# Kernel tuning notes

Measured on AMD Instinct MI355X. Metric: run time of the kernel, lower is better.

## Reference

```python
import jax, jax.numpy as jnp
import numpy as np

N_QUBITS = 8
INPUT_DIM = 256
SEQ_LEN = 256
BATCH = 512


def qgate(theta, x):
    # Closed-form expectation of the PennyLane circuit:
    #   RX(x_i) then RY(theta_i) on each wire (from |0>), then CNOT chain 0->1->...->n-1,
    #   measure <Z_k>.  Single-wire <Z_j> = cos(x_j) * cos(theta_j); CNOT chain maps
    #   Z_k -> Z_0 Z_1 ... Z_k in the Heisenberg picture, so on the product state
    #   <Z_k> = prod_{j<=k} cos(x_j) cos(theta_j).
    # x: (B, n_wires), theta: (n_wires,)
    return jnp.cumprod(jnp.cos(x) * jnp.cos(theta), axis=-1)


def setup_inputs() -> dict:
    key = jax.random.key(0)
    ks = jax.random.split(key, 14)
    d_in = INPUT_DIM + N_QUBITS  # concat([x, hx]) -> 264
    lin_scale = 1.0 / np.sqrt(d_in)
    inp = {
        "inputs": jax.random.normal(ks[0], (SEQ_LEN, BATCH, INPUT_DIM), dtype=jnp.float32),
        "Wf": jax.random.normal(ks[1], (N_QUBITS, d_in), dtype=jnp.float32) * lin_scale,
        "bf": jax.random.normal(ks[2], (N_QUBITS,), dtype=jnp.float32) * lin_scale,
        "Wi": jax.random.normal(ks[3], (N_QUBITS, d_in), dtype=jnp.float32) * lin_scale,
        "bi": jax.random.normal(ks[4], (N_QUBITS,), dtype=jnp.float32) * lin_scale,
        "Wu": jax.random.normal(ks[5], (N_QUBITS, d_in), dtype=jnp.float32) * lin_scale,
        "bu": jax.random.normal(ks[6], (N_QUBITS,), dtype=jnp.float32) * lin_scale,
        "Wo": jax.random.normal(ks[7], (N_QUBITS, d_in), dtype=jnp.float32) * lin_scale,
        "bo": jax.random.normal(ks[8], (N_QUBITS,), dtype=jnp.float32) * lin_scale,
        "pf": jax.random.normal(ks[9], (N_QUBITS,), dtype=jnp.float32),
        "pi_": jax.random.normal(ks[10], (N_QUBITS,), dtype=jnp.float32),
        "pu": jax.random.normal(ks[11], (N_QUBITS,), dtype=jnp.float32),
        "po": jax.random.normal(ks[12], (N_QUBITS,), dtype=jnp.float32),
    }
    return inp


def reference(inputs, Wf, bf, Wi, bi, Wu, bu, Wo, bo, pf, pi_, pu, po):
    B = inputs.shape[1]
    H = pf.shape[0]  # hidden_dim == n_qubits

    def step(carry, x):
        hx, cx = carry
        comb = jnp.concatenate([x, hx], axis=1)  # (B, input_dim + H)
        f = jax.nn.sigmoid(qgate(pf, comb @ Wf.T + bf))
        i = jax.nn.sigmoid(qgate(pi_, comb @ Wi.T + bi))
        g = jnp.tanh(qgate(pu, comb @ Wu.T + bu))
        o = jax.nn.sigmoid(qgate(po, comb @ Wo.T + bo))
        cx = f * cx + i * g
        hx = o * jnp.tanh(cx)
        return (hx, cx), hx

    init = (jnp.zeros((B, H), dtype=inputs.dtype), jnp.zeros((B, H), dtype=inputs.dtype))
    (hx, cx), stacked = jax.lax.scan(step, init, inputs)
    return stacked, hx, cx
```

## Files before the change

### kernel.cpp

```cpp
#include <hip/hip_runtime.h>
#include <hip/hip_bf16.h>


#define SEQ   256
#define BATCH 512
#define DIN   256
#define NROWS (SEQ * BATCH)
#define DCOMB 264
#define CHT   64
#define NCH   (SEQ / CHT)
#define ZBSTR 130
#define ZBUFSZ (32 * ZBSTR + 16)
#define HLSTR 260
#define INV2PI 0.15915494309189535f

typedef __attribute__((ext_vector_type(8))) short short8;
typedef __attribute__((ext_vector_type(4))) float f32x4;
typedef __attribute__((ext_vector_type(2))) float f32x2;

__device__ __forceinline__ short f2bf(float f) {
    union { __hip_bfloat16 h; short s; } u;
    u.h = __float2bfloat16(f);
    return u.s;
}
__device__ __forceinline__ float bf2f(short s) {
    union { short s; __hip_bfloat16 h; } u;
    u.s = s;
    return __bfloat162float(u.h);
}

__device__ __forceinline__ short8 pack8(float4 a, float4 b) {
    union { short8 s8; int i[4]; } u;
    union { __hip_bfloat162 h; int i; } v;
    v.h = __float22bfloat162_rn(make_float2(a.x, a.y)); u.i[0] = v.i;
    v.h = __float22bfloat162_rn(make_float2(a.z, a.w)); u.i[1] = v.i;
    v.h = __float22bfloat162_rn(make_float2(b.x, b.y)); u.i[2] = v.i;
    v.h = __float22bfloat162_rn(make_float2(b.z, b.w)); u.i[3] = v.i;
    return u.s8;
}

#define DPP_ROR(V, S) \
    __int_as_float(__builtin_amdgcn_update_dpp(__float_as_int(V), __float_as_int(V), 0x120 | (S), 0xF, 0xF, false))
#define QP(V, CTRL) \
    __int_as_float(__builtin_amdgcn_update_dpp(__float_as_int(V), __float_as_int(V), (CTRL), 0xF, 0xF, false))
#define PSTG2(A, D) { \
    float s0_ = __int_as_float(__builtin_amdgcn_update_dpp(one_i, __float_as_int(A.x), 0x110 | (D), 0xF, 0xF, false)); \
    float s1_ = __int_as_float(__builtin_amdgcn_update_dpp(one_i, __float_as_int(A.y), 0x110 | (D), 0xF, 0xF, false)); \
    A *= (f32x2){s0_, s1_}; }

__device__ __forceinline__ void scan_body8(
    int T0L, int T0G, const float* __restrict__ zrow,
    float* __restrict__ hlrow, bool writer,
    f32x4 (&ZC)[4], f32x4 (&ZN)[4],
    float& hx, float& cx,
    const f32x2 (&wp)[8], const f32x2 cth,
    const f32x2 k0, const f32x2 k1, const f32x2 k2, const f32x2 k3,
    const f32x2 k4, const int one_i)
{
    #pragma unroll
    for (int j = 0; j < 4; ++j)
        ZN[j] = *(const f32x4*)&zrow[(T0L + 8) * 2 + j * 4];

    float hxh[8];
    #pragma unroll
    for (int u = 0; u < 8; ++u) {
        const f32x2 z2 = (f32x2){ ZC[u >> 1][(u & 1) * 2],
                                  ZC[u >> 1][(u & 1) * 2 + 1] };

        const float h0 = hx;
        const float h1 = DPP_ROR(hx, 2),  h2 = DPP_ROR(hx, 4);
        const float h3 = DPP_ROR(hx, 6),  h4 = DPP_ROR(hx, 8);
        const float h5 = DPP_ROR(hx, 10), h6 = DPP_ROR(hx, 12);
        const float h7 = DPP_ROR(hx, 14);

        f32x2 e0 = (f32x2){h0, h0} * wp[0] + (f32x2){h1, h1} * wp[1];
        f32x2 e1 = (f32x2){h2, h2} * wp[2] + (f32x2){h3, h3} * wp[3];
        f32x2 e2 = (f32x2){h4, h4} * wp[4] + (f32x2){h5, h5} * wp[5];
        f32x2 e3 = (f32x2){h6, h6} * wp[6] + (f32x2){h7, h7} * wp[7];
        const f32x2 p = ((z2 + e0) + (e1 + e2)) + e3;

        f32x2 A = (f32x2){__builtin_amdgcn_cosf(p.x),
                          __builtin_amdgcn_cosf(p.y)} * cth;
        PSTG2(A, 2) PSTG2(A, 4) PSTG2(A, 8)

        const f32x2 t2 = A * A;
        const f32x2 t4 = t2 * t2;
        const f32x2 ra = k1 + t2 * k2;
        const f32x2 rb = k3 + t2 * k4;
        const f32x2 P  = k0 + A * (ra + t4 * rb);

        const float f_all = QP(P.x, 0xA0);
        const float u_all = QP(P.x, 0xF5);
        const float i_all = QP(P.y, 0xA0);
        const float o_all = QP(P.y, 0xF5);

        cx = fmaf(f_all, cx, i_all * u_all);

        const float tq  = cx * cx;
        const float num = cx * fmaf(tq, fmaf(tq, 1.0f, 105.0f), 945.0f);
        const float den = fmaf(tq, fmaf(tq, 15.0f, 420.0f), 945.0f);
        const float tc  = num * __builtin_amdgcn_rcpf(den);

        hx = o_all * tc;
        hxh[u] = hx;
    }

    if (writer) {
        *(f32x4*)&hlrow[T0G]     = (f32x4){hxh[0], hxh[1], hxh[2], hxh[3]};
        *(f32x4*)&hlrow[T0G + 4] = (f32x4){hxh[4], hxh[5], hxh[6], hxh[7]};
    }
}

__global__ __launch_bounds__(512, 1) void qlstm_fused(
    const float* __restrict__ X,
    const float* __restrict__ Wf, const float* __restrict__ Wi,
    const float* __restrict__ Wu, const float* __restrict__ Wo,
    const float* __restrict__ bfv, const float* __restrict__ biv,
    const float* __restrict__ buv, const float* __restrict__ bov,
    const float* __restrict__ pf, const float* __restrict__ pi_,
    const float* __restrict__ pu, const float* __restrict__ po,
    float* __restrict__ out)
{
    __shared__ short8 Wl[2048];
    __shared__ float Zb[2][ZBUFSZ];
    __shared__ float Hl2[16 * HLSTR];

    const int tx  = threadIdx.x;
    const int l   = tx & 63;
    const int wid = tx >> 6;
    const int lm  = l & 15;
    const int lk  = l >> 4;
    const int B0  = blockIdx.x;

    const float* Wg[4] = {Wf, Wi, Wu, Wo};
    const float* Bg[4] = {bfv, biv, buv, bov};

    #pragma unroll
    for (int e = 0; e < 4; ++e) {
        const int ent  = tx + e * 512;
        const int lane = ent & 63;
        const int ks   = (ent >> 6) & 7;
        const int hl   = (ent >> 9) & 1;
        const int nt   = (ent >> 10) & 1;
        const int elm  = lane & 15, elk = lane >> 4;
        const int c    = nt * 16 + elm;
        const float* wrow = Wg[c & 3] + (c >> 2) * DCOMB + ks * 32 + elk * 8;
        short8 fr;
        #pragma unroll
        for (int j = 0; j < 8; ++j) {
            const float v = wrow[j] * INV2PI;
            const short h16 = f2bf(v);
            fr[j] = hl ? f2bf(v - bf2f(h16)) : h16;
        }
        Wl[ent] = fr;
    }

    float bias0, bias1;
    { const int c0 = lm;      bias0 = Bg[c0 & 3][c0 >> 2] * INV2PI;
      const int c1 = 16 + lm; bias1 = Bg[c1 & 3][c1 >> 2] * INV2PI; }

    const int q   = tx & 15;
    const int kq  = q >> 1;
    const int hi  = q & 1;
    const int bl  = (tx >> 4) & 1;
    const int oidx = (B0 * 2 + bl) * 8 + kq;
    const int woff = kq * DCOMB + DIN;

    f32x2 wp[8];
    f32x2 cth = (f32x2){1.0f, 1.0f};
    if (wid == 0) {
        const float* WgA = hi ? Wu : Wf;
        const float* WgB = hi ? Wo : Wi;
        #pragma unroll
        for (int s = 0; s < 8; ++s) {
            const int j = (kq - s) & 7;
            wp[s] = (f32x2){WgA[woff + j] * INV2PI, WgB[woff + j] * INV2PI};
        }
        cth = (f32x2){__cosf((hi ? pu : pf)[kq]),
                      __cosf((hi ? po : pi_)[kq])};
    }
    const float SK1 = 0.25f, SK2 = -0.0208333333f, SK3 = 0.0020833333f,
                SK4 = -0.00021082f;
    const f32x2 k0 = (f32x2){hi ? 0.0f : 0.5f, 0.5f};
    const f32x2 k1 = (f32x2){hi ? 0.9999016f : SK1, SK1};
    const f32x2 k2 = (f32x2){hi ? -0.3310485f : SK2, SK2};
    const f32x2 k3 = (f32x2){hi ? 0.1204423f : SK3, SK3};
    const f32x2 k4 = (f32x2){hi ? -0.0277012f : SK4, SK4};
    const int one_i = __float_as_int(1.0f);

    float hx = 0.0f, cx = 0.0f;
    const float* __restrict__ zrowb = &Zb[0][(bl * 16 + q) * ZBSTR];
    float* __restrict__ hlrow = &Hl2[(bl * 8 + kq) * HLSTR];
    const bool writer = (hi == 0) && (tx < 32);
    f32x4 zbA[4], zbB[4];

    __syncthreads();

    #pragma unroll 1
    for (int k = 0; k <= NCH; ++k) {
        if (wid == 0) {
            if (k >= 1) {
                const float* __restrict__ zrow = zrowb + ((k - 1) & 1) * ZBUFSZ;
                const int TG = (k - 1) * CHT;
                #pragma unroll
                for (int j = 0; j < 4; ++j) zbA[j] = *(const f32x4*)&zrow[j * 4];
                scan_body8( 0, TG,      zrow, hlrow, writer, zbA, zbB, hx, cx, wp, cth, k0, k1, k2, k3, k4, one_i);
                scan_body8( 8, TG + 8,  zrow, hlrow, writer, zbB, zbA, hx, cx, wp, cth, k0, k1, k2, k3, k4, one_i);
                scan_body8(16, TG + 16, zrow, hlrow, writer, zbA, zbB, hx, cx, wp, cth, k0, k1, k2, k3, k4, one_i);
                scan_body8(24, TG + 24, zrow, hlrow, writer, zbB, zbA, hx, cx, wp, cth, k0, k1, k2, k3, k4, one_i);
                scan_body8(32, TG + 32, zrow, hlrow, writer, zbA, zbB, hx, cx, wp, cth, k0, k1, k2, k3, k4, one_i);
                scan_body8(40, TG + 40, zrow, hlrow, writer, zbB, zbA, hx, cx, wp, cth, k0, k1, k2, k3, k4, one_i);
                scan_body8(48, TG + 48, zrow, hlrow, writer, zbA, zbB, hx, cx, wp, cth, k0, k1, k2, k3, k4, one_i);
                scan_body8(56, TG + 56, zrow, hlrow, writer, zbB, zbA, hx, cx, wp, cth, k0, k1, k2, k3, k4, one_i);
                if (k == NCH && writer) {
                    out[NROWS * 8 + oidx]        = hx;
                    out[NROWS * 8 + 4096 + oidx] = cx;
                }
            }
        } else if (wid <= 4 && k < NCH) {
            float* __restrict__ bufp = &Zb[k & 1][0];
            #pragma unroll
            for (int g = 0; g < 2; ++g) {
                const int r0 = k * 128 + (wid - 1) * 32 + g * 16;
                const int r  = r0 + lm;
                const float* xbase =
                    X + ((long)(r >> 1) * BATCH + B0 * 2 + (r & 1)) * DIN + lk * 8;

                float4 xv[16];
                #pragma unroll
                for (int i = 0; i < 16; ++i)
                    xv[i] = *(const float4*)(xbase + (i >> 1) * 32 + (i & 1) * 4);

                f32x4 acc0 = (f32x4){bias0, bias0, bias0, bias0};
                f32x4 acc1 = (f32x4){bias1, bias1, bias1, bias1};
                #pragma unroll
                for (int ks = 0; ks < 8; ++ks) {
                    const short8 a = pack8(xv[2 * ks], xv[2 * ks + 1]);
                    acc0 = __builtin_amdgcn_mfma_f32_16x16x32_bf16(a, Wl[ks * 64 + l],        acc0, 0, 0, 0);
                    acc0 = __builtin_amdgcn_mfma_f32_16x16x32_bf16(a, Wl[(8  + ks) * 64 + l], acc0, 0, 0, 0);
                    acc1 = __builtin_amdgcn_mfma_f32_16x16x32_bf16(a, Wl[(16 + ks) * 64 + l], acc1, 0, 0, 0);
                    acc1 = __builtin_amdgcn_mfma_f32_16x16x32_bf16(a, Wl[(24 + ks) * 64 + l], acc1, 0, 0, 0);
                }

                #pragma unroll
                for (int rr = 0; rr < 4; ++rr) {
                    const int rw   = r0 + lk * 4 + rr;
                    const int tl   = (rw - k * 128) >> 1;
                    const int blw  = rw & 1;
                    bufp[(blw * 16 + (lm >> 1)) * ZBSTR + tl * 2 + (lm & 1)]     = acc0[rr];
                    bufp[(blw * 16 + 8 + (lm >> 1)) * ZBSTR + tl * 2 + (lm & 1)] = acc1[rr];
                }
            }
        }
        __syncthreads();
    }

    {
        const int f0 = tx * 8;
        const int t  = f0 >> 4;
        const int c0 = f0 & 15;
        float4 v0, v1;
        v0.x = Hl2[(c0 + 0) * HLSTR + t];
        v0.y = Hl2[(c0 + 1) * HLSTR + t];
        v0.z = Hl2[(c0 + 2) * HLSTR + t];
        v0.w = Hl2[(c0 + 3) * HLSTR + t];
        v1.x = Hl2[(c0 + 4) * HLSTR + t];
        v1.y = Hl2[(c0 + 5) * HLSTR + t];
        v1.z = Hl2[(c0 + 6) * HLSTR + t];
        v1.w = Hl2[(c0 + 7) * HLSTR + t];
        float4* dst = (float4*)(out + (long)t * (BATCH * 8) + B0 * 16 + c0);
        dst[0] = v0;
        dst[1] = v1;
    }
}

extern "C" void kernel_launch(void* const* d_in, const int* in_sizes, int n_in,
                              void* d_out, int out_size, void* d_ws, size_t ws_size,
                              hipStream_t stream) {
    const float* X   = (const float*)d_in[0];
    const float* Wf  = (const float*)d_in[1];
    const float* bfv = (const float*)d_in[2];
    const float* Wi  = (const float*)d_in[3];
    const float* biv = (const float*)d_in[4];
    const float* Wu  = (const float*)d_in[5];
    const float* buv = (const float*)d_in[6];
    const float* Wo  = (const float*)d_in[7];
    const float* bov = (const float*)d_in[8];
    const float* pf  = (const float*)d_in[9];
    const float* pi_ = (const float*)d_in[10];
    const float* pu  = (const float*)d_in[11];
    const float* po  = (const float*)d_in[12];
    float* out = (float*)d_out;
    (void)d_ws; (void)ws_size;

    qlstm_fused<<<BATCH / 2, 512, 0, stream>>>(
        X, Wf, Wi, Wu, Wo, bfv, biv, buv, bov, pf, pi_, pu, po, out);
}
```

Baseline: 224.5 us.

## Interleave two independent batch recurrences per lane in scan wave

Each lane of the scan wavefront now computes both batch rows' recurrences (A and B) with interleaved steps, instead of each half-wave handling one row. The goal is ILP: two independent dependency chains can hide the latency of DPP, transcendental and rcp instructions on the serial critical path. In exchange each lane does twice the arithmetic and the upper lanes do redundant work. Register pressure also rises from the extra Z buffers and states.

```diff
diff --git a/kernel.cpp b/kernel.cpp
--- a/kernel.cpp
+++ b/kernel.cpp
@@ -48,66 +48,82 @@
     float s1_ = __int_as_float(__builtin_amdgcn_update_dpp(one_i, __float_as_int(A.y), 0x110 | (D), 0xF, 0xF, false)); \
     A *= (f32x2){s0_, s1_}; }
 
-__device__ __forceinline__ void scan_body8(
-    int T0L, int T0G, const float* __restrict__ zrow,
-    float* __restrict__ hlrow, bool writer,
-    f32x4 (&ZC)[4], f32x4 (&ZN)[4],
-    float& hx, float& cx,
+__device__ __forceinline__ float scan_step(
+    const f32x2 z2, float& hx, float& cx,
+    const f32x2 (&wp)[8], const f32x2 cth,
+    const f32x2 k0, const f32x2 k1, const f32x2 k2, const f32x2 k3,
+    const f32x2 k4, const int one_i)
+{
+    const float h0 = hx;
+    const float h1 = DPP_ROR(hx, 2),  h2 = DPP_ROR(hx, 4);
+    const float h3 = DPP_ROR(hx, 6),  h4 = DPP_ROR(hx, 8);
+    const float h5 = DPP_ROR(hx, 10), h6 = DPP_ROR(hx, 12);
+    const float h7 = DPP_ROR(hx, 14);
+
+    f32x2 e0 = (f32x2){h0, h0} * wp[0] + (f32x2){h1, h1} * wp[1];
+    f32x2 e1 = (f32x2){h2, h2} * wp[2] + (f32x2){h3, h3} * wp[3];
+    f32x2 e2 = (f32x2){h4, h4} * wp[4] + (f32x2){h5, h5} * wp[5];
+    f32x2 e3 = (f32x2){h6, h6} * wp[6] + (f32x2){h7, h7} * wp[7];
+    const f32x2 p = ((z2 + e0) + (e1 + e2)) + e3;
+
+    f32x2 A = (f32x2){__builtin_amdgcn_cosf(p.x),
+                      __builtin_amdgcn_cosf(p.y)} * cth;
+    PSTG2(A, 2) PSTG2(A, 4) PSTG2(A, 8)
+
+    const f32x2 t2 = A * A;
+    const f32x2 t4 = t2 * t2;
+    const f32x2 ra = k1 + t2 * k2;
+    const f32x2 rb = k3 + t2 * k4;
+    const f32x2 P  = k0 + A * (ra + t4 * rb);
+
+    const float f_all = QP(P.x, 0xA0);
+    const float u_all = QP(P.x, 0xF5);
+    const float i_all = QP(P.y, 0xA0);
+    const float o_all = QP(P.y, 0xF5);
+
+    cx = fmaf(f_all, cx, i_all * u_all);
+
+    const float tq  = cx * cx;
+    const float num = cx * fmaf(tq, fmaf(tq, 1.0f, 105.0f), 945.0f);
+    const float den = fmaf(tq, fmaf(tq, 15.0f, 420.0f), 945.0f);
+    hx = o_all * (num * __builtin_amdgcn_rcpf(den));
+    return hx;
+}
+
+__device__ __forceinline__ void scan_body8_dual(
+    int T0L, int T0G,
+    const float* __restrict__ zrowA, const float* __restrict__ zrowB,
+    float* __restrict__ hlrow, bool writer, int bl,
+    f32x4 (&ZCa)[4], f32x4 (&ZNa)[4], f32x4 (&ZCb)[4], f32x4 (&ZNb)[4],
+    float& hxA, float& cxA, float& hxB, float& cxB,
     const f32x2 (&wp)[8], const f32x2 cth,
     const f32x2 k0, const f32x2 k1, const f32x2 k2, const f32x2 k3,
     const f32x2 k4, const int one_i)
 {
     #pragma unroll
-    for (int j = 0; j < 4; ++j)
-        ZN[j] = *(const f32x4*)&zrow[(T0L + 8) * 2 + j * 4];
-
-    float hxh[8];
+    for (int j = 0; j < 4; ++j) {
+        ZNa[j] = *(const f32x4*)&zrowA[(T0L + 8) * 2 + j * 4];
+        ZNb[j] = *(const f32x4*)&zrowB[(T0L + 8) * 2 + j * 4];
+    }
+
+    float ha[8], hb[8];
     #pragma unroll
     for (int u = 0; u < 8; ++u) {
-        const f32x2 z2 = (f32x2){ ZC[u >> 1][(u & 1) * 2],
-                                  ZC[u >> 1][(u & 1) * 2 + 1] };
-
-        const float h0 = hx;
-        const float h1 = DPP_ROR(hx, 2),  h2 = DPP_ROR(hx, 4);
-        const float h3 = DPP_ROR(hx, 6),  h4 = DPP_ROR(hx, 8);
-        const float h5 = DPP_ROR(hx, 10), h6 = DPP_ROR(hx, 12);
-        const float h7 = DPP_ROR(hx, 14);
-
-        f32x2 e0 = (f32x2){h0, h0} * wp[0] + (f32x2){h1, h1} * wp[1];
-        f32x2 e1 = (f32x2){h2, h2} * wp[2] + (f32x2){h3, h3} * wp[3];
-        f32x2 e2 = (f32x2){h4, h4} * wp[4] + (f32x2){h5, h5} * wp[5];
-        f32x2 e3 = (f32x2){h6, h6} * wp[6] + (f32x2){h7, h7} * wp[7];
-        const f32x2 p = ((z2 + e0) + (e1 + e2)) + e3;
-
-        f32x2 A = (f32x2){__builtin_amdgcn_cosf(p.x),
-                          __builtin_amdgcn_cosf(p.y)} * cth;
-        PSTG2(A, 2) PSTG2(A, 4) PSTG2(A, 8)
-
-        const f32x2 t2 = A * A;
-        const f32x2 t4 = t2 * t2;
-        const f32x2 ra = k1 + t2 * k2;
-        const f32x2 rb = k3 + t2 * k4;
-        const f32x2 P  = k0 + A * (ra + t4 * rb);
-
-        const float f_all = QP(P.x, 0xA0);
-        const float u_all = QP(P.x, 0xF5);
-        const float i_all = QP(P.y, 0xA0);
-        const float o_all = QP(P.y, 0xF5);
-
-        cx = fmaf(f_all, cx, i_all * u_all);
-
-        const float tq  = cx * cx;
-        const float num = cx * fmaf(tq, fmaf(tq, 1.0f, 105.0f), 945.0f);
-        const float den = fmaf(tq, fmaf(tq, 15.0f, 420.0f), 945.0f);
-        const float tc  = num * __builtin_amdgcn_rcpf(den);
-
-        hx = o_all * tc;
-        hxh[u] = hx;
+        const f32x2 z2a = (f32x2){ ZCa[u >> 1][(u & 1) * 2],
+                                   ZCa[u >> 1][(u & 1) * 2 + 1] };
+        const f32x2 z2b = (f32x2){ ZCb[u >> 1][(u & 1) * 2],
+                                   ZCb[u >> 1][(u & 1) * 2 + 1] };
+        ha[u] = scan_step(z2a, hxA, cxA, wp, cth, k0, k1, k2, k3, k4, one_i);
+        hb[u] = scan_step(z2b, hxB, cxB, wp, cth, k0, k1, k2, k3, k4, one_i);
     }
 
     if (writer) {
-        *(f32x4*)&hlrow[T0G]     = (f32x4){hxh[0], hxh[1], hxh[2], hxh[3]};
-        *(f32x4*)&hlrow[T0G + 4] = (f32x4){hxh[4], hxh[5], hxh[6], hxh[7]};
+        const f32x4 v0 = bl ? (f32x4){hb[0], hb[1], hb[2], hb[3]}
+                            : (f32x4){ha[0], ha[1], ha[2], ha[3]};
+        const f32x4 v1 = bl ? (f32x4){hb[4], hb[5], hb[6], hb[7]}
+                            : (f32x4){ha[4], ha[5], ha[6], ha[7]};
+        *(f32x4*)&hlrow[T0G]     = v0;
+        *(f32x4*)&hlrow[T0G + 4] = v1;
     }
 }
 
@@ -163,7 +179,6 @@
     const int kq  = q >> 1;
     const int hi  = q & 1;
     const int bl  = (tx >> 4) & 1;
-    const int oidx = (B0 * 2 + bl) * 8 + kq;
     const int woff = kq * DCOMB + DIN;
 
     f32x2 wp[8];
@@ -188,11 +203,12 @@
     const f32x2 k4 = (f32x2){hi ? -0.0277012f : SK4, SK4};
     const int one_i = __float_as_int(1.0f);
 
-    float hx = 0.0f, cx = 0.0f;
-    const float* __restrict__ zrowb = &Zb[0][(bl * 16 + q) * ZBSTR];
+    float hxA = 0.0f, cxA = 0.0f, hxB = 0.0f, cxB = 0.0f;
+    const float* __restrict__ zrAbase = &Zb[0][q * ZBSTR];
+    const float* __restrict__ zrBbase = &Zb[0][(16 + q) * ZBSTR];
     float* __restrict__ hlrow = &Hl2[(bl * 8 + kq) * HLSTR];
     const bool writer = (hi == 0) && (tx < 32);
-    f32x4 zbA[4], zbB[4];
+    f32x4 rAa[4], rBa[4], rAb[4], rBb[4];
 
     __syncthreads();
 
@@ -200,21 +216,26 @@
     for (int k = 0; k <= NCH; ++k) {
         if (wid == 0) {
             if (k >= 1) {
-                const float* __restrict__ zrow = zrowb + ((k - 1) & 1) * ZBUFSZ;
+                const float* __restrict__ zA = zrAbase + ((k - 1) & 1) * ZBUFSZ;
+                const float* __restrict__ zB = zrBbase + ((k - 1) & 1) * ZBUFSZ;
                 const int TG = (k - 1) * CHT;
                 #pragma unroll
-                for (int j = 0; j < 4; ++j) zbA[j] = *(const f32x4*)&zrow[j * 4];
-                scan_body8( 0, TG,      zrow, hlrow, writer, zbA, zbB, hx, cx, wp, cth, k0, k1, k2, k3, k4, one_i);
-                scan_body8( 8, TG + 8,  zrow, hlrow, writer, zbB, zbA, hx, cx, wp, cth, k0, k1, k2, k3, k4, one_i);
-                scan_body8(16, TG + 16, zrow, hlrow, writer, zbA, zbB, hx, cx, wp, cth, k0, k1, k2, k3, k4, one_i);
-                scan_body8(24, TG + 24, zrow, hlrow, writer, zbB, zbA, hx, cx, wp, cth, k0, k1, k2, k3, k4, one_i);
-                scan_body8(32, TG + 32, zrow, hlrow, writer, zbA, zbB, hx, cx, wp, cth, k0, k1, k2, k3, k4, one_i);
-                scan_body8(40, TG + 40, zrow, hlrow, writer, zbB, zbA, hx, cx, wp, cth, k0, k1, k2, k3, k4, one_i);
-                scan_body8(48, TG + 48, zrow, hlrow, writer, zbA, zbB, hx, cx, wp, cth, k0, k1, k2, k3, k4, one_i);
-                scan_body8(56, TG + 56, zrow, hlrow, writer, zbB, zbA, hx, cx, wp, cth, k0, k1, k2, k3, k4, one_i);
+                for (int j = 0; j < 4; ++j) {
+                    rAa[j] = *(const f32x4*)&zA[j * 4];
+                    rAb[j] = *(const f32x4*)&zB[j * 4];
+                }
+                scan_body8_dual( 0, TG,      zA, zB, hlrow, writer, bl, rAa, rBa, rAb, rBb, hxA, cxA, hxB, cxB, wp, cth, k0, k1, k2, k3, k4, one_i);
+                scan_body8_dual( 8, TG + 8,  zA, zB, hlrow, writer, bl, rBa, rAa, rBb, rAb, hxA, cxA, hxB, cxB, wp, cth, k0, k1, k2, k3, k4, one_i);
+                scan_body8_dual(16, TG + 16, zA, zB, hlrow, writer, bl, rAa, rBa, rAb, rBb, hxA, cxA, hxB, cxB, wp, cth, k0, k1, k2, k3, k4, one_i);
+                scan_body8_dual(24, TG + 24, zA, zB, hlrow, writer, bl, rBa, rAa, rBb, rAb, hxA, cxA, hxB, cxB, wp, cth, k0, k1, k2, k3, k4, one_i);
+                scan_body8_dual(32, TG + 32, zA, zB, hlrow, writer, bl, rAa, rBa, rAb, rBb, hxA, cxA, hxB, cxB, wp, cth, k0, k1, k2, k3, k4, one_i);
+                scan_body8_dual(40, TG + 40, zA, zB, hlrow, writer, bl, rBa, rAa, rBb, rAb, hxA, cxA, hxB, cxB, wp, cth, k0, k1, k2, k3, k4, one_i);
+                scan_body8_dual(48, TG + 48, zA, zB, hlrow, writer, bl, rAa, rBa, rAb, rBb, hxA, cxA, hxB, cxB, wp, cth, k0, k1, k2, k3, k4, one_i);
+                scan_body8_dual(56, TG + 56, zA, zB, hlrow, writer, bl, rBa, rAa, rBb, rAb, hxA, cxA, hxB, cxB, wp, cth, k0, k1, k2, k3, k4, one_i);
                 if (k == NCH && writer) {
-                    out[NROWS * 8 + oidx]        = hx;
-                    out[NROWS * 8 + 4096 + oidx] = cx;
+                    const int oidx = (B0 * 2 + bl) * 8 + kq;
+                    out[NROWS * 8 + oidx]        = bl ? hxB : hxA;
+                    out[NROWS * 8 + 4096 + oidx] = bl ? cxB : cxA;
                 }
             }
         } else if (wid <= 4 && k < NCH) {
```

Measured after the change: 250.4 us. 11.5% more time.
